# Performance work log

Measured on AMD Instinct MI355X. Metric: run time of the kernel, lower is better.

Reference implementation:

```python
import jax, jax.numpy as jnp
import numpy as np

B, S, D = 128, 512, 240
E, TOP_K = 8, 2


def setup_inputs() -> dict:
    key = jax.random.key(0)
    k1, k2, k3 = jax.random.split(key, 3)
    x = jax.random.normal(k1, (B, S, D), dtype=jnp.float32)
    gate_w = jax.random.normal(k2, (D, E), dtype=jnp.float32) * 0.02
    gate_b = jnp.zeros((E,), dtype=jnp.float32)
    # torch Linear weight is [out, in]; store as [E, D_out, D_in]
    expert_w = jax.random.normal(k3, (E, D, D), dtype=jnp.float32) * 0.02
    expert_b = jnp.zeros((E, D), dtype=jnp.float32)
    return {"x": x, "gate_w": gate_w, "gate_b": gate_b,
            "expert_w": expert_w, "expert_b": expert_b}


def reference(x, gate_w, gate_b, expert_w, expert_b):
    # Gating
    gate_logits = jnp.einsum('bsd,de->bse', x, gate_w) + gate_b      # [B,S,E]
    gate_weights = jax.nn.softmax(gate_logits, axis=-1)
    top_w, top_idx = jax.lax.top_k(gate_weights, TOP_K)              # [B,S,K]
    top_w = top_w / jnp.sum(top_w, axis=-1, keepdims=True)
    # Combine weights per expert: [B,S,E]
    combine = jnp.sum(jax.nn.one_hot(top_idx, E, dtype=x.dtype) * top_w[..., None], axis=-2)
    # Dense all-expert compute (same math as masked dispatch):
    # expert_out[b,s,e,f] = x[b,s,:] @ expert_w[e].T + expert_b[e]
    expert_out = jnp.einsum('bsd,efd->bsef', x, expert_w) + expert_b  # [B,S,E,D]
    out = jnp.einsum('bsef,bse->bsf', expert_out, combine)            # [B,S,D]
    return out
```

## Files before the change

### kernel.cpp

```cpp
#include <hip/hip_runtime.h>
#include <cstdint>

#define NTOK 65536
#define DIM 240
#define KP 256
#define NMETA 576
#define NGB 512

typedef short bf16x8 __attribute__((ext_vector_type(8)));
typedef float f32x16 __attribute__((ext_vector_type(16)));

union U16B { uint4 u; bf16x8 v; };

__device__ __forceinline__ unsigned short f2bf(float x) {
  unsigned int u = __float_as_uint(x);
  u += 0x7fffu + ((u >> 16) & 1u);
  return (unsigned short)(u >> 16);
}

template<int CTRL>
__device__ __forceinline__ float dppf(float v) {
  return __int_as_float(__builtin_amdgcn_update_dpp(0, __float_as_int(v), CTRL, 0xF, 0xF, true));
}
template<int CTRL>
__device__ __forceinline__ unsigned dppu(unsigned v) {
  return (unsigned)__builtin_amdgcn_update_dpp(0, (int)v, CTRL, 0xF, 0xF, true);
}
__device__ __forceinline__ bool pgt(unsigned a, unsigned b) {
  float fa = __uint_as_float(a & ~7u), fb = __uint_as_float(b & ~7u);
  return (fa != fb) ? (fa > fb) : ((a & 7u) < (b & 7u));
}
template<int CTRL>
__device__ __forceinline__ void top2round(unsigned& a1, unsigned& a2) {
  unsigned b1 = dppu<CTRL>(a1), b2 = dppu<CTRL>(a2);
  bool g = pgt(a1, b1);
  unsigned n1 = g ? a1 : b1;
  unsigned lo = g ? b1 : a1;
  unsigned m2 = pgt(a2, b2) ? a2 : b2;
  a2 = pgt(lo, m2) ? lo : m2;
  a1 = n1;
}

__global__ __launch_bounds__(256) void prep_w(const float* __restrict__ ew,
                                              const float* __restrict__ eb,
                                              unsigned short* __restrict__ Wb) {
  int idx = blockIdx.x * 256 + threadIdx.x;
  int k0 = (idx & 63) << 2;
  int n  = (idx >> 6) & 255;
  int e  = idx >> 14;
  ushort4 v = {0, 0, 0, 0};
  if (n < DIM && k0 < DIM) {
    const float* wrow = ew + (e * DIM + n) * DIM;
    v.x = f2bf(wrow[k0]); v.y = f2bf(wrow[k0 + 1]);
    v.z = f2bf(wrow[k0 + 2]); v.w = f2bf(wrow[k0 + 3]);
  }
  *(ushort4*)&Wb[(size_t)idx * 4] = v;
}

__global__ __launch_bounds__(512) void gating(const float* __restrict__ x,
                                              const float* __restrict__ gw,
                                              const float* __restrict__ gb,
                                              unsigned short* __restrict__ xb,
                                              unsigned char* __restrict__ pairid,
                                              float2* __restrict__ wpair,
                                              int* __restrict__ hist2d) {
  __shared__ __align__(16) float gwT[8][DIM];
  __shared__ int hist[64];
  for (int i = threadIdx.x; i < 8 * DIM; i += 512) gwT[i & 7][i >> 3] = gw[i];
  if (threadIdx.x < 64) hist[threadIdx.x] = 0;
  __syncthreads();
  const int lane = threadIdx.x & 63;
  const int w = threadIdx.x >> 6;
  const bool act = lane < 60;
  float4 g[8];
#pragma unroll
  for (int e = 0; e < 8; ++e)
    g[e] = act ? *(const float4*)(&gwT[e][lane * 4]) : make_float4(0.f, 0.f, 0.f, 0.f);
  const int elane = 4 * (lane & 1) + 2 * ((lane >> 1) & 1) + ((lane >> 3) & 1);
  const float gbl = gb[elane];
  const int tbase = blockIdx.x * 128 + w * 16;
  for (int it = 0; it < 16; ++it) {
    const int t = tbase + it;
    float4 xv = act ? *(const float4*)(x + (size_t)t * DIM + lane * 4)
                    : make_float4(0.f, 0.f, 0.f, 0.f);
    float p[8];
#pragma unroll
    for (int e = 0; e < 8; ++e)
      p[e] = xv.x * g[e].x + xv.y * g[e].y + xv.z * g[e].z + xv.w * g[e].w;
    float q4[4];
#pragma unroll
    for (int i = 0; i < 4; ++i) {
      float lo = p[i] + dppf<0xB1>(p[i]);
      float hi = p[i + 4] + dppf<0xB1>(p[i + 4]);
      q4[i] = (lane & 1) ? hi : lo;
    }
    float q2[2];
#pragma unroll
    for (int i = 0; i < 2; ++i) {
      float lo = q4[i] + dppf<0x4E>(q4[i]);
      float hi = q4[i + 2] + dppf<0x4E>(q4[i + 2]);
      q2[i] = (lane & 2) ? hi : lo;
    }
    {
      float lo = q2[0] + dppf<0x128>(q2[0]);
      float hi = q2[1] + dppf<0x128>(q2[1]);
      float s = (lane & 8) ? hi : lo;
      s += __shfl_xor(s, 4);
      s += __shfl_xor(s, 16);
      s += __shfl_xor(s, 32);
      s += gbl;
      unsigned a1 = (__float_as_uint(s) & ~7u) | (unsigned)elane;
      unsigned a2 = (0xFF800000u & ~7u) | 7u;
      top2round<0xB1>(a1, a2);
      top2round<0x4E>(a1, a2);
      top2round<0x128>(a1, a2);
      const int i1 = a1 & 7, i2 = a2 & 7;
      const float l1 = __uint_as_float(a1 & ~7u), l2 = __uint_as_float(a2 & ~7u);
      const float qq = expf(l2 - l1);
      const float w1 = 1.f / (1.f + qq);
      const float w2 = qq / (1.f + qq);
      ushort4 v = {0, 0, 0, 0};
      if (act) { v.x = f2bf(xv.x); v.y = f2bf(xv.y); v.z = f2bf(xv.z); v.w = f2bf(xv.w); }
      *(ushort4*)(xb + (size_t)t * KP + lane * 4) = v;
      if (lane == 0) {
        const int ea = (i1 < i2) ? i1 : i2, eb2 = (i1 < i2) ? i2 : i1;
        const float wa = (i1 < i2) ? w1 : w2, wb2 = (i1 < i2) ? w2 : w1;
        const int pp = ea * 8 + eb2;
        pairid[t] = (unsigned char)pp;
        wpair[t] = make_float2(wa, wb2);
        atomicAdd(&hist[pp], 1);
      }
    }
  }
  __syncthreads();
  if (threadIdx.x < 64) hist2d[blockIdx.x * 64 + threadIdx.x] = hist[threadIdx.x];
}

__global__ __launch_bounds__(512) void scan1_k(const int* __restrict__ hist2d,
                                               int* __restrict__ lbase2d,
                                               int* __restrict__ cnt) {
  __shared__ int s[NGB];
  const int p = blockIdx.x, tid = threadIdx.x;
  const int v = hist2d[tid * 64 + p];
  s[tid] = v;
  __syncthreads();
  for (int off = 1; off < NGB; off <<= 1) {
    int tv = (tid >= off) ? s[tid - off] : 0;
    __syncthreads();
    s[tid] += tv;
    __syncthreads();
  }
  lbase2d[tid * 64 + p] = s[tid] - v;
  if (tid == NGB - 1) cnt[p] = s[tid];
}

__global__ void scan2_k(const int* __restrict__ cnt, int* __restrict__ start,
                        int4* __restrict__ meta) {
  __shared__ int sc[64], sstart[64], stile[64], stot;
  const int tid = threadIdx.x;
  sc[tid] = cnt[tid];
  __syncthreads();
  if (tid == 0) {
    int a = 0, ta = 0;
    for (int p = 0; p < 64; ++p) { sstart[p] = a; stile[p] = ta; a += sc[p]; ta += (sc[p] + 127) >> 7; }
    stot = ta;
  }
  __syncthreads();
  start[tid] = sstart[tid];
  const int c = sc[tid], e0 = tid >> 3, e1 = tid & 7;
  for (int i = 0; (i << 7) < c; ++i)
    meta[stile[tid] + i] = make_int4(e0, e1, sstart[tid] + (i << 7), min(128, c - (i << 7)));
  for (int j = stot + tid; j < NMETA; j += 64)
    meta[j] = make_int4(0, 0, 0, 0);
}

__global__ __launch_bounds__(128) void route_k(const unsigned char* __restrict__ pairid,
                                               const float2* __restrict__ wpair,
                                               const int* __restrict__ start,
                                               const int* __restrict__ lbase2d,
                                               float2* __restrict__ wsorted,
                                               int* __restrict__ tokord) {
  __shared__ int lcnt[64];
  const int b = blockIdx.x, tid = threadIdx.x;
  if (tid < 64) lcnt[tid] = 0;
  __syncthreads();
  const int t = b * 128 + tid;
  const int p = pairid[t];
  const int rank = atomicAdd(&lcnt[p], 1);
  const int pos = start[p] + lbase2d[b * 64 + p] + rank;
  wsorted[pos] = wpair[t];
  tokord[pos] = t;
}

#define GLDS16(g, l)                                                        \
  __builtin_amdgcn_global_load_lds(                                         \
      (__attribute__((address_space(1))) unsigned int*)(g),                 \
      (__attribute__((address_space(3))) unsigned int*)(l), 16, 0, 0)

__global__ __launch_bounds__(512, 2) void moe_gemm_pair(const unsigned short* __restrict__ xb,
                                                        const unsigned short* __restrict__ Wb,
                                                        const float* __restrict__ ebias,
                                                        const float2* __restrict__ wsorted,
                                                        const int* __restrict__ tokord,
                                                        const int4* __restrict__ meta,
                                                        float* __restrict__ out) {
  extern __shared__ __align__(16) char smem[];
  char* Ab = smem;
  char* Wd = smem + 61440;
  int* ptok = (int*)(smem + 77824);
  float2* wab = (float2*)(smem + 78336);

  const int4 m = meta[blockIdx.x >> 1];
  const int n = m.w;
  if (n == 0) return;
  const int ch = blockIdx.x & 1;
  const int tid = threadIdx.x, lane = tid & 63, wid = tid >> 6;
  const int wr = wid >> 2, wcl = wid & 3;
  const int l31 = lane & 31, hi = lane >> 5;

  if (tid < 128) {
    const int idx = m.z + (tid < n ? tid : n - 1);
    ptok[tid] = tokord[idx];
    wab[tid] = wsorted[idx];
  }
  __syncthreads();

  const int se = (tid >> 7) & 1;
  const char* wsrc = (const char*)Wb
      + (size_t)((se ? m.y : m.x) * 256 + ch * 128 + (tid & 127)) * 512
      + (tid >> 8) * 16;

#pragma unroll
  for (int j = 0; j < 7; ++j) {
    const int i = j * 512 + tid;
    GLDS16((const char*)xb + (size_t)ptok[i & 127] * 512 + (i >> 7) * 16, Ab + i * 16);
  }
  if (tid < 256) {
    const int i = 3584 + tid;
    GLDS16((const char*)xb + (size_t)ptok[i & 127] * 512 + (i >> 7) * 16, Ab + i * 16);
  }
  GLDS16(wsrc, Wd + tid * 16);
  __syncthreads();

  f32x16 acc[2][2] = {};

  for (int it = 0; it < 15; ++it) {
    const int buf = it & 1;
    if (it < 14) GLDS16(wsrc + (it + 1) * 32, Wd + ((buf ^ 1) << 13) + tid * 16);
    const char* Ar = Ab + ((2 * it + hi) << 11);
    const char* Wg = Wd + (buf << 13) + (hi << 12) + ((wcl * 32 + l31) << 4);
    U16B a0, a1, b0, b1;
    a0.u = *(const uint4*)(Ar + ((wr * 64 + l31) << 4));
    a1.u = *(const uint4*)(Ar + ((wr * 64 + 32 + l31) << 4));
    b0.u = *(const uint4*)(Wg);
    b1.u = *(const uint4*)(Wg + 2048);
    acc[0][0] = __builtin_amdgcn_mfma_f32_32x32x16_bf16(a0.v, b0.v, acc[0][0], 0, 0, 0);
    acc[0][1] = __builtin_amdgcn_mfma_f32_32x32x16_bf16(a1.v, b0.v, acc[0][1], 0, 0, 0);
    acc[1][0] = __builtin_amdgcn_mfma_f32_32x32x16_bf16(a0.v, b1.v, acc[1][0], 0, 0, 0);
    acc[1][1] = __builtin_amdgcn_mfma_f32_32x32x16_bf16(a1.v, b1.v, acc[1][1], 0, 0, 0);
    __syncthreads();
  }

  const int col = ch * 128 + wcl * 32 + l31;
  if (col < DIM) {
    const float be0 = ebias[m.x * DIM + col];
    const float be1 = ebias[m.y * DIM + col];
#pragma unroll
    for (int af = 0; af < 2; ++af) {
#pragma unroll
      for (int r = 0; r < 16; ++r) {
        const int rw = wr * 64 + af * 32 + (r & 3) + ((r >> 2) << 3) + (hi << 2);
        if (rw < n) {
          const float2 w2 = wab[rw];
          out[(size_t)ptok[rw] * DIM + col] =
              w2.x * (acc[0][af][r] + be0) + w2.y * (acc[1][af][r] + be1);
        }
      }
    }
  }
}

extern "C" void kernel_launch(void* const* d_in, const int* in_sizes, int n_in,
                              void* d_out, int out_size, void* d_ws, size_t ws_size,
                              hipStream_t stream) {
  const float* x  = (const float*)d_in[0];
  const float* gw = (const float*)d_in[1];
  const float* gb = (const float*)d_in[2];
  const float* ew = (const float*)d_in[3];
  const float* eb = (const float*)d_in[4];
  float* out = (float*)d_out;

  char* ws = (char*)d_ws;
  unsigned short* Wb   = (unsigned short*)ws;
  unsigned short* xb   = (unsigned short*)(ws + 1048576);
  float2*         wpr  = (float2*)(ws + 34603008);
  float2*         wsr  = (float2*)(ws + 35127296);
  int*            tord = (int*)(ws + 35651584);
  unsigned char*  pid  = (unsigned char*)(ws + 35913728);
  int*            h2d  = (int*)(ws + 35979264);
  int*            lb2d = (int*)(ws + 36110336);
  int*            cnt  = (int*)(ws + 36241408);
  int*            strt = (int*)(ws + 36241664);
  int4*           meta = (int4*)(ws + 36241920);

  hipFuncSetAttribute((const void*)moe_gemm_pair, hipFuncAttributeMaxDynamicSharedMemorySize, 79360);

  prep_w<<<512, 256, 0, stream>>>(ew, eb, Wb);
  gating<<<NGB, 512, 0, stream>>>(x, gw, gb, xb, pid, wpr, h2d);
  scan1_k<<<64, NGB, 0, stream>>>(h2d, lb2d, cnt);
  scan2_k<<<1, 64, 0, stream>>>(cnt, strt, meta);
  route_k<<<NGB, 128, 0, stream>>>(pid, wpr, strt, lb2d, wsr, tord);
  moe_gemm_pair<<<2 * NMETA, 512, 79360, stream>>>(xb, Wb, eb, wsr, tord, meta, out);
}
```

Before: 107.5 us.

## Permute bf16 activations into sorted order and transpose weight layout for GEMM

The bf16 conversion of x moves out of gating into a new permute kernel, which writes each token's row to its sorted slot. The grouped GEMM can then load contiguous A rows with an XOR swizzle instead of gathering by token index. The weight prep writes a k-group-major transposed layout so each pipeline stage's weight slice is contiguous, and the main loop uses explicit vmcnt waits and raw barriers instead of a trailing __syncthreads. In exchange, x is read twice (gating and permute), and the epilogue now reads tokord and wsorted from global memory instead of shared memory.

```diff
diff --git a/kernel.cpp b/kernel.cpp
--- a/kernel.cpp
+++ b/kernel.cpp
@@ -42,8 +42,7 @@
 }
 
 __global__ __launch_bounds__(256) void prep_w(const float* __restrict__ ew,
-                                              const float* __restrict__ eb,
-                                              unsigned short* __restrict__ Wb) {
+                                              unsigned short* __restrict__ WbT) {
   int idx = blockIdx.x * 256 + threadIdx.x;
   int k0 = (idx & 63) << 2;
   int n  = (idx >> 6) & 255;
@@ -54,13 +53,12 @@
     v.x = f2bf(wrow[k0]); v.y = f2bf(wrow[k0 + 1]);
     v.z = f2bf(wrow[k0 + 2]); v.w = f2bf(wrow[k0 + 3]);
   }
-  *(ushort4*)&Wb[(size_t)idx * 4] = v;
+  *(ushort4*)&WbT[((size_t)(e * 32 + (k0 >> 3)) * 256 + n) * 8 + (k0 & 7)] = v;
 }
 
 __global__ __launch_bounds__(512) void gating(const float* __restrict__ x,
                                               const float* __restrict__ gw,
                                               const float* __restrict__ gb,
-                                              unsigned short* __restrict__ xb,
                                               unsigned char* __restrict__ pairid,
                                               float2* __restrict__ wpair,
                                               int* __restrict__ hist2d) {
@@ -101,35 +99,30 @@
       float hi = q4[i + 2] + dppf<0x4E>(q4[i + 2]);
       q2[i] = (lane & 2) ? hi : lo;
     }
-    {
-      float lo = q2[0] + dppf<0x128>(q2[0]);
-      float hi = q2[1] + dppf<0x128>(q2[1]);
-      float s = (lane & 8) ? hi : lo;
-      s += __shfl_xor(s, 4);
-      s += __shfl_xor(s, 16);
-      s += __shfl_xor(s, 32);
-      s += gbl;
-      unsigned a1 = (__float_as_uint(s) & ~7u) | (unsigned)elane;
-      unsigned a2 = (0xFF800000u & ~7u) | 7u;
-      top2round<0xB1>(a1, a2);
-      top2round<0x4E>(a1, a2);
-      top2round<0x128>(a1, a2);
+    float lo = q2[0] + dppf<0x128>(q2[0]);
+    float hi = q2[1] + dppf<0x128>(q2[1]);
+    float s = (lane & 8) ? hi : lo;
+    s += __shfl_xor(s, 4);
+    s += __shfl_xor(s, 16);
+    s += __shfl_xor(s, 32);
+    s += gbl;
+    unsigned a1 = (__float_as_uint(s) & ~7u) | (unsigned)elane;
+    unsigned a2 = (0xFF800000u & ~7u) | 7u;
+    top2round<0xB1>(a1, a2);
+    top2round<0x4E>(a1, a2);
+    top2round<0x128>(a1, a2);
+    if (lane == 0) {
       const int i1 = a1 & 7, i2 = a2 & 7;
       const float l1 = __uint_as_float(a1 & ~7u), l2 = __uint_as_float(a2 & ~7u);
       const float qq = expf(l2 - l1);
       const float w1 = 1.f / (1.f + qq);
       const float w2 = qq / (1.f + qq);
-      ushort4 v = {0, 0, 0, 0};
-      if (act) { v.x = f2bf(xv.x); v.y = f2bf(xv.y); v.z = f2bf(xv.z); v.w = f2bf(xv.w); }
-      *(ushort4*)(xb + (size_t)t * KP + lane * 4) = v;
-      if (lane == 0) {
-        const int ea = (i1 < i2) ? i1 : i2, eb2 = (i1 < i2) ? i2 : i1;
-        const float wa = (i1 < i2) ? w1 : w2, wb2 = (i1 < i2) ? w2 : w1;
-        const int pp = ea * 8 + eb2;
-        pairid[t] = (unsigned char)pp;
-        wpair[t] = make_float2(wa, wb2);
-        atomicAdd(&hist[pp], 1);
-      }
+      const int ea = (i1 < i2) ? i1 : i2, eb2 = (i1 < i2) ? i2 : i1;
+      const float wa = (i1 < i2) ? w1 : w2, wb2 = (i1 < i2) ? w2 : w1;
+      const int pp = ea * 8 + eb2;
+      pairid[t] = (unsigned char)pp;
+      wpair[t] = make_float2(wa, wb2);
+      atomicAdd(&hist[pp], 1);
     }
   }
   __syncthreads();
@@ -174,22 +167,42 @@
     meta[j] = make_int4(0, 0, 0, 0);
 }
 
-__global__ __launch_bounds__(128) void route_k(const unsigned char* __restrict__ pairid,
-                                               const float2* __restrict__ wpair,
-                                               const int* __restrict__ start,
-                                               const int* __restrict__ lbase2d,
-                                               float2* __restrict__ wsorted,
-                                               int* __restrict__ tokord) {
-  __shared__ int lcnt[64];
+__global__ __launch_bounds__(512) void permute_k(const float* __restrict__ x,
+                                                 const unsigned char* __restrict__ pairid,
+                                                 const float2* __restrict__ wpair,
+                                                 const int* __restrict__ start,
+                                                 const int* __restrict__ lbase2d,
+                                                 unsigned short* __restrict__ xbs,
+                                                 float2* __restrict__ wsorted,
+                                                 int* __restrict__ tokord) {
+  __shared__ int lcnt[64], sp[128];
   const int b = blockIdx.x, tid = threadIdx.x;
   if (tid < 64) lcnt[tid] = 0;
   __syncthreads();
-  const int t = b * 128 + tid;
-  const int p = pairid[t];
-  const int rank = atomicAdd(&lcnt[p], 1);
-  const int pos = start[p] + lbase2d[b * 64 + p] + rank;
-  wsorted[pos] = wpair[t];
-  tokord[pos] = t;
+  if (tid < 128) {
+    const int t = b * 128 + tid;
+    const int p = pairid[t];
+    const int rank = atomicAdd(&lcnt[p], 1);
+    const int pos = start[p] + lbase2d[b * 64 + p] + rank;
+    sp[tid] = pos;
+    wsorted[pos] = wpair[t];
+    tokord[pos] = t;
+  }
+  __syncthreads();
+  for (int j = tid; j < 128 * 32; j += 512) {
+    const int tl = j >> 5, og = j & 31;
+    const size_t src = (size_t)(b * 128 + tl) * DIM + og * 8;
+    ushort4 o0 = {0, 0, 0, 0}, o1 = {0, 0, 0, 0};
+    if (og < 30) {
+      const float4 q0 = *(const float4*)(x + src);
+      const float4 q1 = *(const float4*)(x + src + 4);
+      o0.x = f2bf(q0.x); o0.y = f2bf(q0.y); o0.z = f2bf(q0.z); o0.w = f2bf(q0.w);
+      o1.x = f2bf(q1.x); o1.y = f2bf(q1.y); o1.z = f2bf(q1.z); o1.w = f2bf(q1.w);
+    }
+    unsigned short* dst = xbs + (size_t)sp[tl] * KP + og * 8;
+    *(ushort4*)dst = o0;
+    *(ushort4*)(dst + 4) = o1;
+  }
 }
 
 #define GLDS16(g, l)                                                        \
@@ -197,19 +210,14 @@
       (__attribute__((address_space(1))) unsigned int*)(g),                 \
       (__attribute__((address_space(3))) unsigned int*)(l), 16, 0, 0)
 
-__global__ __launch_bounds__(512, 2) void moe_gemm_pair(const unsigned short* __restrict__ xb,
-                                                        const unsigned short* __restrict__ Wb,
+__global__ __launch_bounds__(512, 2) void moe_gemm_pair(const unsigned short* __restrict__ xbs,
+                                                        const unsigned short* __restrict__ WbT,
                                                         const float* __restrict__ ebias,
                                                         const float2* __restrict__ wsorted,
                                                         const int* __restrict__ tokord,
                                                         const int4* __restrict__ meta,
                                                         float* __restrict__ out) {
   extern __shared__ __align__(16) char smem[];
-  char* Ab = smem;
-  char* Wd = smem + 61440;
-  int* ptok = (int*)(smem + 77824);
-  float2* wab = (float2*)(smem + 78336);
-
   const int4 m = meta[blockIdx.x >> 1];
   const int n = m.w;
   if (n == 0) return;
@@ -218,47 +226,52 @@
   const int wr = wid >> 2, wcl = wid & 3;
   const int l31 = lane & 31, hi = lane >> 5;
 
-  if (tid < 128) {
-    const int idx = m.z + (tid < n ? tid : n - 1);
-    ptok[tid] = tokord[idx];
-    wab[tid] = wsorted[idx];
-  }
-  __syncthreads();
-
-  const int se = (tid >> 7) & 1;
-  const char* wsrc = (const char*)Wb
-      + (size_t)((se ? m.y : m.x) * 256 + ch * 128 + (tid & 127)) * 512
-      + (tid >> 8) * 16;
-
-#pragma unroll
-  for (int j = 0; j < 7; ++j) {
-    const int i = j * 512 + tid;
-    GLDS16((const char*)xb + (size_t)ptok[i & 127] * 512 + (i >> 7) * 16, Ab + i * 16);
-  }
-  if (tid < 256) {
-    const int i = 3584 + tid;
-    GLDS16((const char*)xb + (size_t)ptok[i & 127] * 512 + (i >> 7) * 16, Ab + i * 16);
-  }
-  GLDS16(wsrc, Wd + tid * 16);
+#pragma unroll
+  for (int j = 0; j < 8; ++j) {
+    const int o = tid * 16 + j * 8192;
+    const int row = o >> 9, gl = (o >> 4) & 31;
+    GLDS16((const char*)xbs + (size_t)(m.z + row) * 512 + ((gl ^ (row & 31)) << 4),
+           smem + o);
+  }
+  const int sg = tid >> 8, se = (tid >> 7) & 1, scol = tid & 127;
+  const char* wsrc0 = (const char*)WbT + (size_t)(se ? m.y : m.x) * 131072
+                    + (size_t)sg * 4096 + (size_t)(ch * 128 + scol) * 16;
+  char* wlds = smem + 65536;
+  GLDS16(wsrc0, wlds + tid * 16);
   __syncthreads();
 
   f32x16 acc[2][2] = {};
+  const int rA0 = wr * 64 + l31, rA1 = rA0 + 32;
+  const char* wrd = wlds + (hi << 12) + ((wcl * 32 + l31) << 4);
 
   for (int it = 0; it < 15; ++it) {
     const int buf = it & 1;
-    if (it < 14) GLDS16(wsrc + (it + 1) * 32, Wd + ((buf ^ 1) << 13) + tid * 16);
-    const char* Ar = Ab + ((2 * it + hi) << 11);
-    const char* Wg = Wd + (buf << 13) + (hi << 12) + ((wcl * 32 + l31) << 4);
+    if (it > 0) {
+      __builtin_amdgcn_s_barrier();
+      __builtin_amdgcn_sched_barrier(0);
+    }
+    if (it < 14) {
+      GLDS16(wsrc0 + (size_t)(it + 1) * 8192, wlds + ((buf ^ 1) << 13) + tid * 16);
+      __builtin_amdgcn_sched_barrier(0);
+      asm volatile("s_waitcnt vmcnt(1)" ::: "memory");
+    } else {
+      asm volatile("s_waitcnt vmcnt(0)" ::: "memory");
+    }
+    __builtin_amdgcn_sched_barrier(0);
+    __builtin_amdgcn_s_barrier();
+    __builtin_amdgcn_sched_barrier(0);
+
+    const int G = 2 * it + hi;
     U16B a0, a1, b0, b1;
-    a0.u = *(const uint4*)(Ar + ((wr * 64 + l31) << 4));
-    a1.u = *(const uint4*)(Ar + ((wr * 64 + 32 + l31) << 4));
-    b0.u = *(const uint4*)(Wg);
-    b1.u = *(const uint4*)(Wg + 2048);
+    a0.u = *(const uint4*)(smem + rA0 * 512 + ((G ^ l31) << 4));
+    a1.u = *(const uint4*)(smem + rA1 * 512 + ((G ^ l31) << 4));
+    const char* wp = wrd + (buf << 13);
+    b0.u = *(const uint4*)(wp);
+    b1.u = *(const uint4*)(wp + 2048);
     acc[0][0] = __builtin_amdgcn_mfma_f32_32x32x16_bf16(a0.v, b0.v, acc[0][0], 0, 0, 0);
     acc[0][1] = __builtin_amdgcn_mfma_f32_32x32x16_bf16(a1.v, b0.v, acc[0][1], 0, 0, 0);
     acc[1][0] = __builtin_amdgcn_mfma_f32_32x32x16_bf16(a0.v, b1.v, acc[1][0], 0, 0, 0);
     acc[1][1] = __builtin_amdgcn_mfma_f32_32x32x16_bf16(a1.v, b1.v, acc[1][1], 0, 0, 0);
-    __syncthreads();
   }
 
   const int col = ch * 128 + wcl * 32 + l31;
@@ -271,8 +284,9 @@
       for (int r = 0; r < 16; ++r) {
         const int rw = wr * 64 + af * 32 + (r & 3) + ((r >> 2) << 3) + (hi << 2);
         if (rw < n) {
-          const float2 w2 = wab[rw];
-          out[(size_t)ptok[rw] * DIM + col] =
+          const int t = tokord[m.z + rw];
+          const float2 w2 = wsorted[m.z + rw];
+          out[(size_t)t * DIM + col] =
               w2.x * (acc[0][af][r] + be0) + w2.y * (acc[1][af][r] + be1);
         }
       }
@@ -291,24 +305,24 @@
   float* out = (float*)d_out;
 
   char* ws = (char*)d_ws;
-  unsigned short* Wb   = (unsigned short*)ws;
-  unsigned short* xb   = (unsigned short*)(ws + 1048576);
-  float2*         wpr  = (float2*)(ws + 34603008);
-  float2*         wsr  = (float2*)(ws + 35127296);
-  int*            tord = (int*)(ws + 35651584);
-  unsigned char*  pid  = (unsigned char*)(ws + 35913728);
-  int*            h2d  = (int*)(ws + 35979264);
-  int*            lb2d = (int*)(ws + 36110336);
-  int*            cnt  = (int*)(ws + 36241408);
-  int*            strt = (int*)(ws + 36241664);
-  int4*           meta = (int4*)(ws + 36241920);
-
-  hipFuncSetAttribute((const void*)moe_gemm_pair, hipFuncAttributeMaxDynamicSharedMemorySize, 79360);
-
-  prep_w<<<512, 256, 0, stream>>>(ew, eb, Wb);
-  gating<<<NGB, 512, 0, stream>>>(x, gw, gb, xb, pid, wpr, h2d);
+  unsigned short* WbT  = (unsigned short*)ws;
+  unsigned short* xbs  = (unsigned short*)(ws + 1048576);
+  float2*         wpr  = (float2*)(ws + 34734080);
+  float2*         wsr  = (float2*)(ws + 35258368);
+  int*            tord = (int*)(ws + 35784704);
+  unsigned char*  pid  = (unsigned char*)(ws + 36047872);
+  int*            h2d  = (int*)(ws + 36113408);
+  int*            lb2d = (int*)(ws + 36244480);
+  int*            cnt  = (int*)(ws + 36375552);
+  int*            strt = (int*)(ws + 36375808);
+  int4*           meta = (int4*)(ws + 36376064);
+
+  hipFuncSetAttribute((const void*)moe_gemm_pair, hipFuncAttributeMaxDynamicSharedMemorySize, 81920);
+
+  prep_w<<<512, 256, 0, stream>>>(ew, WbT);
+  gating<<<NGB, 512, 0, stream>>>(x, gw, gb, pid, wpr, h2d);
   scan1_k<<<64, NGB, 0, stream>>>(h2d, lb2d, cnt);
   scan2_k<<<1, 64, 0, stream>>>(cnt, strt, meta);
-  route_k<<<NGB, 128, 0, stream>>>(pid, wpr, strt, lb2d, wsr, tord);
-  moe_gemm_pair<<<2 * NMETA, 512, 79360, stream>>>(xb, Wb, eb, wsr, tord, meta, out);
-}
+  permute_k<<<NGB, 512, 0, stream>>>(x, pid, wpr, strt, lb2d, xbs, wsr, tord);
+  moe_gemm_pair<<<2 * NMETA, 512, 81920, stream>>>(xbs, WbT, eb, wsr, tord, meta, out);
+}
```

After: 115.1 us. 7.1% more time.
